# Kernel tuning notes

Measured on AMD Instinct MI355X. Metric: run time of the kernel, lower is better.

Reference implementation:

```python
import jax, jax.numpy as jnp
import numpy as np

DIM = 256
HEADS = 8
DIM_HEAD = 32
AGENT = 6
WIN = 7


def _relative_position_index(L, Wh, Ww):
    coords = np.stack(np.meshgrid(np.arange(L), np.arange(Wh), np.arange(Ww), indexing='ij'))
    cf = coords.reshape(3, -1)                      # (3, N)
    rel = cf[:, :, None] - cf[:, None, :]           # (3, N, N)
    rel = rel.transpose(1, 2, 0).astype(np.int64)   # (N, N, 3)
    rel[..., 0] += L - 1
    rel[..., 1] += Wh - 1
    rel[..., 2] += Ww - 1
    rel[..., 0] *= (2 * Wh - 1) * (2 * Ww - 1)
    rel[..., 1] *= 2 * Ww - 1
    return rel.sum(-1)                              # (N, N)


def setup_inputs() -> dict:
    key = jax.random.key(0)
    k1, k2, k3, k4, k5 = jax.random.split(key, 5)
    B, X, Y = 2, 8, 8
    x = jax.random.normal(k1, (B, AGENT, X, Y, WIN, WIN, DIM), dtype=jnp.float32)
    mask = jax.random.randint(k2, (B, X, Y, WIN, WIN, 1, AGENT), 0, 2, dtype=jnp.int32)
    w_qkv = jax.random.normal(k3, (3 * DIM, DIM), dtype=jnp.float32) * 0.02
    w_out = jax.random.normal(k4, (DIM, DIM), dtype=jnp.float32) * 0.02
    n_bias = (2 * AGENT - 1) * (2 * WIN - 1) * (2 * WIN - 1)
    bias_table = jax.random.normal(k5, (n_bias, HEADS), dtype=jnp.float32) * 0.02
    return {"x": x, "mask": mask, "w_qkv": w_qkv, "w_out": w_out, "bias_table": bias_table}


def reference(x, mask, w_qkv, w_out, bias_table):
    B, L, X, Y, W1, W2, C = x.shape
    h, dh = HEADS, DIM_HEAD
    N = L * W1 * W2
    scale = dh ** -0.5

    # 'b l x y w1 w2 d -> (b x y) (l w1 w2) d'
    xr = jnp.transpose(x, (0, 2, 3, 1, 4, 5, 6)).reshape(B * X * Y, N, C)

    qkv = jnp.einsum('bnc,ec->bne', xr, w_qkv)      # (Bw, N, 3C)
    q, k, v = jnp.split(qkv, 3, axis=-1)
    def to_heads(t):
        return jnp.transpose(t.reshape(B * X * Y, N, h, dh), (0, 2, 1, 3))
    q, k, v = to_heads(q) * scale, to_heads(k), to_heads(v)

    sim = jnp.einsum('bhid,bhjd->bhij', q, k)       # (Bw, h, N, N)

    rel_idx = jnp.asarray(_relative_position_index(L, W1, W2))
    bias = bias_table[rel_idx]                      # (N, N, h)
    sim = sim + jnp.transpose(bias, (2, 0, 1))[None]

    # 'b x y w1 w2 e l -> (b x y) e (l w1 w2)'
    m = jnp.transpose(mask, (0, 1, 2, 5, 6, 3, 4)).reshape(B * X * Y, 1, N)
    sim = jnp.where(m[:, :, None, :] == 0, jnp.float32(-1e9), sim)

    attn = jax.nn.softmax(sim, axis=-1)
    out = jnp.einsum('bhij,bhjd->bhid', attn, v)    # (Bw, h, N, dh)

    # 'b h (l w1 w2) d -> b l w1 w2 (h d)'
    out = jnp.transpose(out, (0, 2, 1, 3)).reshape(B * X * Y, L, W1, W2, C)
    out = jnp.einsum('blwvc,ec->blwve', out, w_out)

    # '(b x y) l w1 w2 d -> b l x y w1 w2 d'
    out = out.reshape(B, X, Y, L, W1, W2, C)
    return jnp.transpose(out, (0, 3, 1, 2, 4, 5, 6))
```

## Files before the change

### kernel.cpp

```cpp
#include <hip/hip_runtime.h>
#include <hip/hip_bf16.h>

#define DIM 256
#define HEADS 8
#define DH 32
#define AGENT 6
#define WIN 7
#define NTOK 294
#define BWIN 128
#define SCALE 0.17677669529663687f
#define LOG2E 1.4426950408889634f
#define TP 19
#define QSTR 40
#define PSTR 320

typedef __hip_bfloat16 bf16;
typedef __attribute__((ext_vector_type(8))) short s16x8;
typedef __attribute__((ext_vector_type(4))) float f32x4;
typedef __attribute__((ext_vector_type(4))) unsigned int u32x4;

#if __has_builtin(__builtin_amdgcn_exp2f)
#define EXP2(x) __builtin_amdgcn_exp2f(x)
#else
#define EXP2(x) exp2f(x)
#endif

__device__ __forceinline__ float bfv(unsigned short u){ return __uint_as_float(((unsigned int)u) << 16); }
__device__ __forceinline__ unsigned short f2bu(float f){
    bf16 b = __float2bfloat16(f); return *reinterpret_cast<unsigned short*>(&b);
}
__device__ __forceinline__ float rdf(const void* p, size_t idx, int isf32) {
    return isf32 ? ((const float*)p)[idx] : bfv(((const unsigned short*)p)[idx]);
}

__device__ __forceinline__ int vtswz(int d, int cByte) {
    return (d * (PSTR * 2) + cByte) ^ (((d >> 1) & 7) << 4);
}

__device__ __forceinline__ void gll16(const void* gp, void* lp) {
    __builtin_amdgcn_global_load_lds(
        (const __attribute__((address_space(1))) unsigned int*)gp,
        (__attribute__((address_space(3))) unsigned int*)lp, 16, 0, 0);
}

__device__ __forceinline__ int detect_flag(const unsigned short* __restrict__ xraw,
                                           int* sflag, int nthreads) {
    if (threadIdx.x == 0) *sflag = 0;
    __syncthreads();
    int bad = 0;
    for (int i = threadIdx.x; i < 8192; i += nthreads) {
        float v = bfv(xraw[i]);
        if (!(fabsf(v) <= 1e10f)) bad = 1;
    }
    if (bad) atomicOr(sflag, 1);
    __syncthreads();
    return *sflag;
}

__global__ __launch_bounds__(256) void prep_kernel(
    const unsigned short* __restrict__ xraw,
    const void* __restrict__ wq, const void* __restrict__ wo, const void* __restrict__ bt,
    unsigned short* __restrict__ Wq, unsigned short* __restrict__ Wo,
    unsigned short* __restrict__ biasB) {
    __shared__ int sflag;
    const int isf32 = detect_flag(xraw, &sflag, 256);
    const int bid = blockIdx.x;
    if (bid < 722) {
        int idx = bid * 256 + threadIdx.x;
        int lane = idx & 63; int t = idx >> 6;
        int jt = t % TP; t /= TP; int it = t % TP; int h = t / TP;
        int i = it * 16 + (lane & 15);
        int g = lane >> 4;
        ushort4 v;
        unsigned short* vp = (unsigned short*)&v;
        #pragma unroll
        for (int r = 0; r < 4; r++) {
            int j = jt * 16 + g * 4 + r;
            float val = 0.f;
            if (i < NTOK && j < NTOK) {
                int li = i / 49, ri = i - li * 49, w1i = ri / 7, w2i = ri - w1i * 7;
                int lj = j / 49, rj = j - lj * 49, w1j = rj / 7, w2j = rj - w1j * 7;
                int rel = (li - lj + AGENT - 1) * 169 + (w1i - w1j + WIN - 1) * 13 + (w2i - w2j + WIN - 1);
                val = rdf(bt, (size_t)rel * HEADS + h, isf32) * LOG2E;
            }
            vp[r] = f2bu(val);
        }
        ((ushort4*)biasB)[idx] = v;
    } else {
        int c = (bid - 722) * 256 + threadIdx.x;
        const void* src; unsigned short* dst; size_t off;
        if (c < 24576) { src = wq; dst = Wq; off = (size_t)c * 8; }
        else           { src = wo; dst = Wo; off = (size_t)(c - 24576) * 8; }
        if (isf32) {
            const float4* s4 = (const float4*)((const float*)src + off);
            float4 v0 = s4[0], v1 = s4[1];
            s16x8 u;
            u[0] = (short)f2bu(v0.x); u[1] = (short)f2bu(v0.y); u[2] = (short)f2bu(v0.z); u[3] = (short)f2bu(v0.w);
            u[4] = (short)f2bu(v1.x); u[5] = (short)f2bu(v1.y); u[6] = (short)f2bu(v1.z); u[7] = (short)f2bu(v1.w);
            *(s16x8*)(dst + off) = u;
        } else {
            *(uint4*)(dst + off) = *(const uint4*)((const unsigned short*)src + off);
        }
    }
}

__device__ __forceinline__ void stage64_g(const unsigned short* __restrict__ g,
                                          unsigned short* lds, size_t rowBase) {
    const int lane = threadIdx.x & 63, wv = threadIdx.x >> 6;
    const int sub = lane >> 5;
    const int colB = (lane & 31) << 4;
    #pragma unroll
    for (int k = 0; k < 8; k++) {
        const int rr = (wv * 8 + k) * 2 + sub;
        const int cg = colB ^ ((rr & 7) << 4);
        gll16((const char*)g + (rowBase + (size_t)rr) * 512 + cg,
              lds + (size_t)(wv * 8 + k) * 512);
    }
}

__device__ __forceinline__ void stage64_f(const float* __restrict__ g,
                                          unsigned short* lds, size_t rowBase) {
    const int tid = threadIdx.x;
    #pragma unroll
    for (int k = 0; k < 8; k++) {
        int ch = k * 256 + tid;
        int rr = ch >> 5;
        int cB = (ch & 31) << 4;
        int cg = cB ^ ((rr & 7) << 4);
        const f32x4* s4 = (const f32x4*)(g + (rowBase + (size_t)rr) * 256 + (cg >> 1));
        f32x4 v0 = __builtin_nontemporal_load(s4);
        f32x4 v1 = __builtin_nontemporal_load(s4 + 1);
        s16x8 u;
        u[0] = (short)f2bu(v0[0]); u[1] = (short)f2bu(v0[1]); u[2] = (short)f2bu(v0[2]); u[3] = (short)f2bu(v0[3]);
        u[4] = (short)f2bu(v1[0]); u[5] = (short)f2bu(v1[1]); u[6] = (short)f2bu(v1[2]); u[7] = (short)f2bu(v1[3]);
        *(s16x8*)(lds + (size_t)rr * 256 + (cB >> 1)) = u;
    }
}

__global__ __launch_bounds__(256) void qkv_mfma(
    const void* __restrict__ xin, const unsigned short* __restrict__ Wq,
    bf16* __restrict__ Q, bf16* __restrict__ K, bf16* __restrict__ V) {
    __shared__ unsigned short P0[64 * 256];
    __shared__ unsigned short P1[64 * 256];
    __shared__ int sflag;
    const int isf32 = detect_flag((const unsigned short*)xin, &sflag, 256);
    const size_t mBase = (size_t)blockIdx.x * 64;
    if (isf32) stage64_f((const float*)xin, P1, mBase);
    else       stage64_g((const unsigned short*)xin, P1, mBase);
    stage64_g(Wq, P0, 0);
    const int tid = threadIdx.x;
    const int wave = tid >> 6, lane = tid & 63;
    const int li = lane & 15, g = lane >> 4;
    const int wm = wave & 1, wn = wave >> 1;
    unsigned int rowOff[2][4];
    #pragma unroll
    for (int mi = 0; mi < 2; mi++)
        #pragma unroll
        for (int r = 0; r < 4; r++) {
            unsigned int m = (unsigned int)mBase + wm * 32 + mi * 16 + g * 4 + r;
            unsigned int w2 = m % 7u, t1 = m / 7u;
            unsigned int w1 = t1 % 7u, t2 = t1 / 7u;
            unsigned int yy = t2 & 7u, t3 = t2 >> 3;
            unsigned int xx = t3 & 7u, t4 = t3 >> 3;
            unsigned int l = t4 % 6u, b = t4 / 6u;
            unsigned int bw = (b << 6) | (xx << 3) | yy;
            unsigned int n = l * 49u + w1 * 7u + w2;
            rowOff[mi][r] = bw * 75264u + n * 32u;
        }
    const int koX = (li & 7) * 8;
    __syncthreads();
    s16x8 a0r[8], a1r[8];
    #pragma unroll
    for (int kc = 0; kc < 8; kc++) {
        const int ko = (kc * 32 + g * 8) ^ koX;
        a0r[kc] = *(const s16x8*)&P1[(wm * 32 + li) * 256 + ko];
        a1r[kc] = *(const s16x8*)&P1[(wm * 32 + 16 + li) * 256 + ko];
    }
    __syncthreads();
    for (int c = 0; c < 12; c++) {
        const unsigned short* Bc = (c & 1) ? P1 : P0;
        unsigned short* Bn = (c & 1) ? P0 : P1;
        if (c + 1 < 12) stage64_g(Wq, Bn, (size_t)(c + 1) * 64);
        f32x4 acc[2][2];
        #pragma unroll
        for (int mi = 0; mi < 2; mi++)
            #pragma unroll
            for (int ni = 0; ni < 2; ni++) acc[mi][ni] = (f32x4){0.f, 0.f, 0.f, 0.f};
        #pragma unroll
        for (int kc = 0; kc < 8; kc++) {
            const int ko = (kc * 32 + g * 8) ^ koX;
            s16x8 b0 = *(const s16x8*)&Bc[(wn * 32 + li) * 256 + ko];
            s16x8 b1 = *(const s16x8*)&Bc[(wn * 32 + 16 + li) * 256 + ko];
            acc[0][0] = __builtin_amdgcn_mfma_f32_16x16x32_bf16(a0r[kc], b0, acc[0][0], 0, 0, 0);
            acc[0][1] = __builtin_amdgcn_mfma_f32_16x16x32_bf16(a0r[kc], b1, acc[0][1], 0, 0, 0);
            acc[1][0] = __builtin_amdgcn_mfma_f32_16x16x32_bf16(a1r[kc], b0, acc[1][0], 0, 0, 0);
            acc[1][1] = __builtin_amdgcn_mfma_f32_16x16x32_bf16(a1r[kc], b1, acc[1][1], 0, 0, 0);
        }
        const int p = c >> 2;
        bf16* dst = (p == 0) ? Q : (p == 1) ? K : V;
        const float sc = (p == 0) ? (SCALE * LOG2E) : 1.0f;
        const unsigned int hoff = ((c & 3) * 2 + wn) * 9408u;
        #pragma unroll
        for (int ni = 0; ni < 2; ni++) {
            const unsigned int d = ni * 16 + li;
            #pragma unroll
            for (int mi = 0; mi < 2; mi++)
                #pragma unroll
                for (int r = 0; r < 4; r++)
                    dst[(size_t)(rowOff[mi][r] + hoff + d)] =
                        __float2bfloat16(acc[mi][ni][r] * sc);
        }
        __syncthreads();
    }
}

__global__ __launch_bounds__(512, 2) void attn_mfma(
    const bf16* __restrict__ Q, const bf16* __restrict__ K, const bf16* __restrict__ V,
    const unsigned short* __restrict__ biasB, const int* __restrict__ mask,
    bf16* __restrict__ AT) {
    __shared__ unsigned short Ks[304 * QSTR];
    __shared__ unsigned short Vt[32 * PSTR];
    __shared__ int ms[320];
    const int tid = threadIdx.x;
    const int bw = blockIdx.x >> 3, h = blockIdx.x & 7;
    const size_t base = ((size_t)bw * HEADS + h) * NTOK * DH;
    const unsigned int* Kg = (const unsigned int*)(K + base);
    const unsigned int* Vg = (const unsigned int*)(V + base);
    const unsigned short* Qg = (const unsigned short*)(Q + base);
    char* VtB = (char*)Vt;
    for (int gg = tid; gg < NTOK * DH / 2; gg += 512) {
        int r = gg >> 4, d2 = (gg & 15) * 2;
        unsigned int uk = __builtin_nontemporal_load(&Kg[gg]);
        unsigned int uv = __builtin_nontemporal_load(&Vg[gg]);
        *(unsigned int*)&Ks[r * QSTR + d2] = uk;
        *(unsigned short*)(VtB + vtswz(d2,     r * 2)) = (unsigned short)(uv & 0xffffu);
        *(unsigned short*)(VtB + vtswz(d2 + 1, r * 2)) = (unsigned short)(uv >> 16);
    }
    for (int e = NTOK * QSTR + tid; e < 304 * QSTR; e += 512) { Ks[e] = 0; }
    for (int idx = tid; idx < 32 * (PSTR - NTOK); idx += 512) {
        int d = idx / (PSTR - NTOK), c = NTOK + idx % (PSTR - NTOK);
        *(unsigned short*)(VtB + vtswz(d, c * 2)) = 0;
    }
    for (int j = tid; j < 320; j += 512) {
        int mv = 0;
        if (j < NTOK) { int a = j / 49, jr = j - a * 49; mv = mask[((size_t)bw * 49 + jr) * AGENT + a]; }
        ms[j] = mv;
    }
    __syncthreads();
    const int wave = tid >> 6, lane = tid & 63;
    const int li = lane & 15, g = lane >> 4;
    unsigned int mb0 = 0, mb1 = 0, mb2 = 0;
    for (int jt = 0; jt < TP; jt++)
        for (int r = 0; r < 4; r++) {
            int j = jt * 16 + g * 4 + r;
            if (j < NTOK && ms[j]) {
                int bit = jt * 4 + r;
                if (bit < 32) mb0 |= (1u << bit);
                else if (bit < 64) mb1 |= (1u << (bit - 32));
                else mb2 |= (1u << (bit - 64));
            }
        }
    const ushort4* bb = (const ushort4*)biasB + (size_t)h * TP * TP * 64;
    const int sAg = li + ((lane & 16) << 1);
    const int sBg = sAg + 16;
    const bool hiSel = (lane >= 32);
    for (int it = wave; it < TP; it += 8) {
        const s16x8 bq = *(const s16x8*)&Qg[((size_t)it * 16 + li) * DH + g * 8];
        f32x4 s[TP];
        __builtin_amdgcn_s_setprio(1);
        #pragma unroll
        for (int jt = 0; jt < TP; jt++) {
            ushort4 bv = bb[(it * TP + jt) * 64 + lane];
            f32x4 c = {bfv(bv.x), bfv(bv.y), bfv(bv.z), bfv(bv.w)};
            s16x8 ak = *(const s16x8*)&Ks[(jt * 16 + li) * QSTR + g * 8];
            s[jt] = __builtin_amdgcn_mfma_f32_16x16x32_bf16(ak, bq, c, 0, 0, 0);
        }
        __builtin_amdgcn_s_setprio(0);
        float mx = -INFINITY;
        #pragma unroll
        for (int jt = 0; jt < TP; jt++)
            #pragma unroll
            for (int r = 0; r < 4; r++) {
                int bit = jt * 4 + r;
                unsigned int w = (bit < 32) ? mb0 : (bit < 64) ? mb1 : mb2;
                float sv = ((w >> (bit & 31)) & 1u) ? s[jt][r] : -1e9f;
                if (jt == TP - 1 && g * 4 + r >= 6) sv = -INFINITY;
                s[jt][r] = sv;
                mx = fmaxf(mx, sv);
            }
        mx = fmaxf(mx, __shfl_xor(mx, 16));
        mx = fmaxf(mx, __shfl_xor(mx, 32));
        float sum = 0.f;
        unsigned int p0[TP], p1[TP];
        #pragma unroll
        for (int jt = 0; jt < TP; jt++) {
            float e0 = EXP2(s[jt][0] - mx);
            float e1 = EXP2(s[jt][1] - mx);
            float e2 = EXP2(s[jt][2] - mx);
            float e3 = EXP2(s[jt][3] - mx);
            sum += (e0 + e1) + (e2 + e3);
            unsigned int lo, hi;
            asm("v_cvt_pk_bf16_f32 %0, %1, %2" : "=v"(lo) : "v"(e0), "v"(e1));
            asm("v_cvt_pk_bf16_f32 %0, %1, %2" : "=v"(hi) : "v"(e2), "v"(e3));
            p0[jt] = lo; p1[jt] = hi;
        }
        sum += __shfl_xor(sum, 16);
        sum += __shfl_xor(sum, 32);
        const float inv = 1.0f / sum;
        f32x4 o0 = {0.f, 0.f, 0.f, 0.f}, o1 = {0.f, 0.f, 0.f, 0.f};
        #pragma unroll
        for (int kc = 0; kc < 10; kc++) {
            unsigned int a0q = __shfl(p0[2 * kc], sAg);
            unsigned int b0q = __shfl(p1[2 * kc], sAg);
            unsigned int c0q = __shfl(p0[2 * kc], sBg);
            unsigned int d0q = __shfl(p1[2 * kc], sBg);
            unsigned int a1q = 0, b1q = 0, c1q = 0, d1q = 0;
            if (2 * kc + 1 < TP) {
                a1q = __shfl(p0[2 * kc + 1], sAg);
                b1q = __shfl(p1[2 * kc + 1], sAg);
                c1q = __shfl(p0[2 * kc + 1], sBg);
                d1q = __shfl(p1[2 * kc + 1], sBg);
            }
            u32x4 w;
            w[0] = hiSel ? a1q : a0q;
            w[1] = hiSel ? b1q : b0q;
            w[2] = hiSel ? c1q : c0q;
            w[3] = hiSel ? d1q : d0q;
            s16x8 ap = __builtin_bit_cast(s16x8, w);
            s16x8 b0 = *(const s16x8*)(VtB + vtswz(li,      (kc * 32 + g * 8) * 2));
            s16x8 b1 = *(const s16x8*)(VtB + vtswz(li + 16, (kc * 32 + g * 8) * 2));
            __builtin_amdgcn_s_setprio(1);
            o0 = __builtin_amdgcn_mfma_f32_16x16x32_bf16(ap, b0, o0, 0, 0, 0);
            o1 = __builtin_amdgcn_mfma_f32_16x16x32_bf16(ap, b1, o1, 0, 0, 0);
            __builtin_amdgcn_s_setprio(0);
        }
        #pragma unroll
        for (int r = 0; r < 4; r++) {
            float iv = __shfl(inv, g * 4 + r);
            int i = it * 16 + g * 4 + r;
            if (i < NTOK) {
                size_t ob = ((size_t)bw * NTOK + i) * DIM + h * DH;
                AT[ob + li]      = __float2bfloat16(o0[r] * iv);
                AT[ob + 16 + li] = __float2bfloat16(o1[r] * iv);
            }
        }
    }
}

__global__ __launch_bounds__(256) void proj_mfma(
    const bf16* __restrict__ AT, const unsigned short* __restrict__ Wo,
    float* __restrict__ out) {
    __shared__ unsigned short P0[64 * 256];
    __shared__ unsigned short P1[64 * 256];
    const size_t mBase = (size_t)blockIdx.x * 64;
    stage64_g((const unsigned short*)AT, P1, mBase);
    stage64_g(Wo, P0, 0);
    const int tid = threadIdx.x;
    const int wave = tid >> 6, lane = tid & 63;
    const int li = lane & 15, g = lane >> 4;
    const int wm = wave & 1, wn = wave >> 1;
    unsigned int offO[2][4];
    #pragma unroll
    for (int mi = 0; mi < 2; mi++)
        #pragma unroll
        for (int r = 0; r < 4; r++) {
            unsigned int m = (unsigned int)mBase + wm * 32 + mi * 16 + g * 4 + r;
            unsigned int bw = m / 294u, n = m - bw * 294u;
            unsigned int b = bw >> 6, xx = (bw >> 3) & 7u, yy = bw & 7u;
            unsigned int l = n / 49u, rr = n - l * 49u, w1 = rr / 7u, w2 = rr - w1 * 7u;
            offO[mi][r] = ((((((b * 6u + l) * 8u + xx) * 8u + yy) * 7u + w1) * 7u) + w2) * 256u;
        }
    const int koX = (li & 7) * 8;
    __syncthreads();
    s16x8 a0r[8], a1r[8];
    #pragma unroll
    for (int kc = 0; kc < 8; kc++) {
        const int ko = (kc * 32 + g * 8) ^ koX;
        a0r[kc] = *(const s16x8*)&P1[(wm * 32 + li) * 256 + ko];
        a1r[kc] = *(const s16x8*)&P1[(wm * 32 + 16 + li) * 256 + ko];
    }
    __syncthreads();
    for (int ec = 0; ec < 4; ec++) {
        const unsigned short* Bc = (ec & 1) ? P1 : P0;
        unsigned short* Bn = (ec & 1) ? P0 : P1;
        if (ec + 1 < 4) stage64_g(Wo, Bn, (size_t)(ec + 1) * 64);
        f32x4 acc[2][2];
        #pragma unroll
        for (int mi = 0; mi < 2; mi++)
            #pragma unroll
            for (int ni = 0; ni < 2; ni++) acc[mi][ni] = (f32x4){0.f, 0.f, 0.f, 0.f};
        #pragma unroll
        for (int kc = 0; kc < 8; kc++) {
            const int ko = (kc * 32 + g * 8) ^ koX;
            s16x8 b0 = *(const s16x8*)&Bc[(wn * 32 + li) * 256 + ko];
            s16x8 b1 = *(const s16x8*)&Bc[(wn * 32 + 16 + li) * 256 + ko];
            acc[0][0] = __builtin_amdgcn_mfma_f32_16x16x32_bf16(a0r[kc], b0, acc[0][0], 0, 0, 0);
            acc[0][1] = __builtin_amdgcn_mfma_f32_16x16x32_bf16(a0r[kc], b1, acc[0][1], 0, 0, 0);
            acc[1][0] = __builtin_amdgcn_mfma_f32_16x16x32_bf16(a1r[kc], b0, acc[1][0], 0, 0, 0);
            acc[1][1] = __builtin_amdgcn_mfma_f32_16x16x32_bf16(a1r[kc], b1, acc[1][1], 0, 0, 0);
        }
        #pragma unroll
        for (int ni = 0; ni < 2; ni++) {
            const unsigned int e = ec * 64 + wn * 32 + ni * 16 + li;
            #pragma unroll
            for (int mi = 0; mi < 2; mi++)
                #pragma unroll
                for (int r = 0; r < 4; r++)
                    __builtin_nontemporal_store(acc[mi][ni][r],
                        &out[(size_t)(offO[mi][r] + e)]);
        }
        __syncthreads();
    }
}

extern "C" void kernel_launch(void* const* d_in, const int* in_sizes, int n_in,
                              void* d_out, int out_size, void* d_ws, size_t ws_size,
                              hipStream_t stream) {
    const long long SZ_X = 9633792, SZ_M = 37632, SZ_WQ = 196608, SZ_WO = 65536, SZ_BT = 14872;
    const void* x = d_in[0]; const void* maskp = d_in[1]; const void* wqkv = d_in[2];
    const void* wout = d_in[3]; const void* btab = d_in[4];
    for (int i = 0; i < n_in; i++) {
        long long s = in_sizes[i];
        if (s == SZ_X) x = d_in[i];
        else if (s == SZ_M) maskp = d_in[i];
        else if (s == SZ_WQ) wqkv = d_in[i];
        else if (s == SZ_WO) wout = d_in[i];
        else if (s == SZ_BT) btab = d_in[i];
    }
    const int* mask = (const int*)maskp;
    float* out = (float*)d_out;
    const size_t SZ = (size_t)BWIN * NTOK * DIM;
    bf16* Q  = (bf16*)d_ws;
    bf16* K  = Q + SZ;
    bf16* V  = K + SZ;
    bf16* AT = V + SZ;
    unsigned short* biasB = (unsigned short*)(AT + SZ);
    const size_t NBB = (size_t)HEADS * TP * TP * 64 * 4;
    unsigned short* Wq = biasB + NBB;
    unsigned short* Wo = Wq + 196608;
    prep_kernel<<<dim3(850), dim3(256), 0, stream>>>(
        (const unsigned short*)x, wqkv, wout, btab, Wq, Wo, biasB);
    qkv_mfma<<<dim3(588), dim3(256), 0, stream>>>(x, Wq, Q, K, V);
    attn_mfma<<<dim3(BWIN * HEADS), dim3(512), 0, stream>>>(Q, K, V, biasB, mask, AT);
    proj_mfma<<<dim3(588), dim3(256), 0, stream>>>(AT, Wo, out);
}
```

Measured before the change: 208.8 us.

## Split attention row into two online-softmax halves to raise occupancy to 3 blocks

Restructures the per-wave attention loop to process the 19 key tiles in two chunks of 10 and 9, using an online softmax with running max and rescaling of the output accumulators. This cuts live score and probability registers roughly in half. The launch-bounds hint goes from 2 to 3 blocks per CU to get more latency hiding. The cost is extra exp, shuffle and rescale work per chunk, plus possible spills if the tighter register budget is not met.

```diff
diff --git a/kernel.cpp b/kernel.cpp
--- a/kernel.cpp
+++ b/kernel.cpp
@@ -214,7 +214,7 @@
     }
 }
 
-__global__ __launch_bounds__(512, 2) void attn_mfma(
+__global__ __launch_bounds__(512, 3) void attn_mfma(
     const bf16* __restrict__ Q, const bf16* __restrict__ K, const bf16* __restrict__ V,
     const unsigned short* __restrict__ biasB, const int* __restrict__ mask,
     bf16* __restrict__ AT) {
@@ -266,74 +266,95 @@
     const bool hiSel = (lane >= 32);
     for (int it = wave; it < TP; it += 8) {
         const s16x8 bq = *(const s16x8*)&Qg[((size_t)it * 16 + li) * DH + g * 8];
-        f32x4 s[TP];
-        __builtin_amdgcn_s_setprio(1);
-        #pragma unroll
-        for (int jt = 0; jt < TP; jt++) {
-            ushort4 bv = bb[(it * TP + jt) * 64 + lane];
-            f32x4 c = {bfv(bv.x), bfv(bv.y), bfv(bv.z), bfv(bv.w)};
-            s16x8 ak = *(const s16x8*)&Ks[(jt * 16 + li) * QSTR + g * 8];
-            s[jt] = __builtin_amdgcn_mfma_f32_16x16x32_bf16(ak, bq, c, 0, 0, 0);
-        }
-        __builtin_amdgcn_s_setprio(0);
-        float mx = -INFINITY;
-        #pragma unroll
-        for (int jt = 0; jt < TP; jt++)
+        float m_run = -INFINITY, sum = 0.f;
+        f32x4 o0 = {0.f, 0.f, 0.f, 0.f}, o1 = {0.f, 0.f, 0.f, 0.f};
+        #pragma unroll
+        for (int half = 0; half < 2; half++) {
+            const int jt0 = half * 10;
+            const int NT = half ? 9 : 10;
+            f32x4 s[10];
+            __builtin_amdgcn_s_setprio(1);
+            #pragma unroll
+            for (int j = 0; j < 10; j++) {
+                if (j >= NT) break;
+                int jt = jt0 + j;
+                ushort4 bv = bb[(it * TP + jt) * 64 + lane];
+                f32x4 c = {bfv(bv.x), bfv(bv.y), bfv(bv.z), bfv(bv.w)};
+                s16x8 ak = *(const s16x8*)&Ks[(jt * 16 + li) * QSTR + g * 8];
+                s[j] = __builtin_amdgcn_mfma_f32_16x16x32_bf16(ak, bq, c, 0, 0, 0);
+            }
+            __builtin_amdgcn_s_setprio(0);
+            float mloc = -INFINITY;
+            #pragma unroll
+            for (int j = 0; j < 10; j++) {
+                if (j >= NT) break;
+                #pragma unroll
+                for (int r = 0; r < 4; r++) {
+                    int bit = (jt0 + j) * 4 + r;
+                    unsigned int w = (bit < 32) ? mb0 : (bit < 64) ? mb1 : mb2;
+                    float sv = ((w >> (bit & 31)) & 1u) ? s[j][r] : -1e9f;
+                    if (jt0 + j == TP - 1 && g * 4 + r >= 6) sv = -INFINITY;
+                    s[j][r] = sv;
+                    mloc = fmaxf(mloc, sv);
+                }
+            }
+            mloc = fmaxf(mloc, __shfl_xor(mloc, 16));
+            mloc = fmaxf(mloc, __shfl_xor(mloc, 32));
+            const float mnew = fmaxf(m_run, mloc);
+            const float scale = EXP2(m_run - mnew);
+            sum *= scale;
             #pragma unroll
             for (int r = 0; r < 4; r++) {
-                int bit = jt * 4 + r;
-                unsigned int w = (bit < 32) ? mb0 : (bit < 64) ? mb1 : mb2;
-                float sv = ((w >> (bit & 31)) & 1u) ? s[jt][r] : -1e9f;
-                if (jt == TP - 1 && g * 4 + r >= 6) sv = -INFINITY;
-                s[jt][r] = sv;
-                mx = fmaxf(mx, sv);
-            }
-        mx = fmaxf(mx, __shfl_xor(mx, 16));
-        mx = fmaxf(mx, __shfl_xor(mx, 32));
-        float sum = 0.f;
-        unsigned int p0[TP], p1[TP];
-        #pragma unroll
-        for (int jt = 0; jt < TP; jt++) {
-            float e0 = EXP2(s[jt][0] - mx);
-            float e1 = EXP2(s[jt][1] - mx);
-            float e2 = EXP2(s[jt][2] - mx);
-            float e3 = EXP2(s[jt][3] - mx);
-            sum += (e0 + e1) + (e2 + e3);
-            unsigned int lo, hi;
-            asm("v_cvt_pk_bf16_f32 %0, %1, %2" : "=v"(lo) : "v"(e0), "v"(e1));
-            asm("v_cvt_pk_bf16_f32 %0, %1, %2" : "=v"(hi) : "v"(e2), "v"(e3));
-            p0[jt] = lo; p1[jt] = hi;
+                const float sc_r = __shfl(scale, g * 4 + r);
+                o0[r] *= sc_r;
+                o1[r] *= sc_r;
+            }
+            m_run = mnew;
+            unsigned int p0[10], p1[10];
+            p0[9] = 0; p1[9] = 0;
+            float lsum = 0.f;
+            #pragma unroll
+            for (int j = 0; j < 10; j++) {
+                if (j >= NT) break;
+                float e0 = EXP2(s[j][0] - mnew);
+                float e1 = EXP2(s[j][1] - mnew);
+                float e2 = EXP2(s[j][2] - mnew);
+                float e3 = EXP2(s[j][3] - mnew);
+                lsum += (e0 + e1) + (e2 + e3);
+                unsigned int lo, hi;
+                asm("v_cvt_pk_bf16_f32 %0, %1, %2" : "=v"(lo) : "v"(e0), "v"(e1));
+                asm("v_cvt_pk_bf16_f32 %0, %1, %2" : "=v"(hi) : "v"(e2), "v"(e3));
+                p0[j] = lo; p1[j] = hi;
+            }
+            sum += lsum;
+            #pragma unroll
+            for (int kc = 0; kc < 5; kc++) {
+                const int kcg = half * 5 + kc;
+                unsigned int a0q = __shfl(p0[2 * kc], sAg);
+                unsigned int b0q = __shfl(p1[2 * kc], sAg);
+                unsigned int c0q = __shfl(p0[2 * kc], sBg);
+                unsigned int d0q = __shfl(p1[2 * kc], sBg);
+                unsigned int a1q = __shfl(p0[2 * kc + 1], sAg);
+                unsigned int b1q = __shfl(p1[2 * kc + 1], sAg);
+                unsigned int c1q = __shfl(p0[2 * kc + 1], sBg);
+                unsigned int d1q = __shfl(p1[2 * kc + 1], sBg);
+                u32x4 w;
+                w[0] = hiSel ? a1q : a0q;
+                w[1] = hiSel ? b1q : b0q;
+                w[2] = hiSel ? c1q : c0q;
+                w[3] = hiSel ? d1q : d0q;
+                s16x8 ap = __builtin_bit_cast(s16x8, w);
+                s16x8 b0 = *(const s16x8*)(VtB + vtswz(li,      (kcg * 32 + g * 8) * 2));
+                s16x8 b1 = *(const s16x8*)(VtB + vtswz(li + 16, (kcg * 32 + g * 8) * 2));
+                __builtin_amdgcn_s_setprio(1);
+                o0 = __builtin_amdgcn_mfma_f32_16x16x32_bf16(ap, b0, o0, 0, 0, 0);
+                o1 = __builtin_amdgcn_mfma_f32_16x16x32_bf16(ap, b1, o1, 0, 0, 0);
+                __builtin_amdgcn_s_setprio(0);
+            }
         }
         sum += __shfl_xor(sum, 16);
         sum += __shfl_xor(sum, 32);
         const float inv = 1.0f / sum;
-        f32x4 o0 = {0.f, 0.f, 0.f, 0.f}, o1 = {0.f, 0.f, 0.f, 0.f};
-        #pragma unroll
-        for (int kc = 0; kc < 10; kc++) {
-            unsigned int a0q = __shfl(p0[2 * kc], sAg);
-            unsigned int b0q = __shfl(p1[2 * kc], sAg);
-            unsigned int c0q = __shfl(p0[2 * kc], sBg);
-            unsigned int d0q = __shfl(p1[2 * kc], sBg);
-            unsigned int a1q = 0, b1q = 0, c1q = 0, d1q = 0;
-            if (2 * kc + 1 < TP) {
-                a1q = __shfl(p0[2 * kc + 1], sAg);
-                b1q = __shfl(p1[2 * kc + 1], sAg);
-                c1q = __shfl(p0[2 * kc + 1], sBg);
-                d1q = __shfl(p1[2 * kc + 1], sBg);
-            }
-            u32x4 w;
-            w[0] = hiSel ? a1q : a0q;
-            w[1] = hiSel ? b1q : b0q;
-            w[2] = hiSel ? c1q : c0q;
-            w[3] = hiSel ? d1q : d0q;
-            s16x8 ap = __builtin_bit_cast(s16x8, w);
-            s16x8 b0 = *(const s16x8*)(VtB + vtswz(li,      (kc * 32 + g * 8) * 2));
-            s16x8 b1 = *(const s16x8*)(VtB + vtswz(li + 16, (kc * 32 + g * 8) * 2));
-            __builtin_amdgcn_s_setprio(1);
-            o0 = __builtin_amdgcn_mfma_f32_16x16x32_bf16(ap, b0, o0, 0, 0, 0);
-            o1 = __builtin_amdgcn_mfma_f32_16x16x32_bf16(ap, b1, o1, 0, 0, 0);
-            __builtin_amdgcn_s_setprio(0);
-        }
         #pragma unroll
         for (int r = 0; r < 4; r++) {
             float iv = __shfl(inv, g * 4 + r);
```

Result: slower. 253.6 us (+21.5%).
